# Optimization experiments

Measured on AMD Instinct MI355X. Metric: run time of the kernel, lower is better.

## Reference

```python
import jax, jax.numpy as jnp
import numpy as np
from jax import lax

N = 1_000_000   # nodes
E = 16_000_000  # edges
K1, K2, K3 = 100_000, 10_000, 2_500  # ceil(ratio*n) per pooling stage
EPS = 1e-5


def cgconv(x, src, dst, edge_attr, edge_valid, Wf, bf, Ws, bs, gamma, beta, num_nodes):
    # z_ij = [x_i, x_j, e_ij]  (PyG: i = target = dst, j = source = src)
    z = jnp.concatenate([x[dst], x[src], edge_attr], axis=-1)          # [E,3]
    m = jax.nn.sigmoid(z @ Wf + bf) * jax.nn.softplus(z @ Ws + bs)     # [E,1]
    m = m * edge_valid[:, None].astype(m.dtype)
    aggr = jax.ops.segment_sum(m, dst, num_segments=num_nodes)         # [n,1]
    # BatchNorm1d (training-mode batch stats, biased var), then residual
    mean = aggr.mean(axis=0)
    var = aggr.var(axis=0)
    bn = gamma * (aggr - mean) / jnp.sqrt(var + EPS) + beta
    return bn + x


def topk_pool(x, src, dst, edge_attr, edge_valid, w, k, num_nodes):
    # Original torch code broadcasts x[N,1]*w[C] -> sum(-1) == x*sum(w); tanh nonlinearity.
    score = jnp.tanh(x[:, 0] * jnp.sum(w) / jnp.linalg.norm(w))        # [n]
    top_scores, perm = lax.top_k(score, k)
    x_new = x[perm] * top_scores[:, None]
    mask = jnp.zeros((num_nodes,), bool).at[perm].set(True)
    new_idx = jnp.zeros((num_nodes,), jnp.int32).at[perm].set(jnp.arange(k, dtype=jnp.int32))
    ev = edge_valid & mask[src] & mask[dst]
    return x_new, new_idx[src], new_idx[dst], edge_attr, ev


def setup_inputs() -> dict:
    key = jax.random.key(0)
    ks = jax.random.split(key, 24)
    d = {}
    d["x"] = jax.random.normal(ks[0], (N, 1), jnp.float32)
    d["edge_attr"] = jax.random.uniform(ks[1], (E, 1), jnp.float32)
    d["src"] = jax.random.randint(ks[2], (E,), 0, N, jnp.int32)
    d["dst"] = jax.random.randint(ks[3], (E,), 0, N, jnp.int32)
    d["batch"] = jnp.zeros((N,), jnp.int32)
    p = lambda k, shp: jax.random.normal(k, shp, jnp.float32) * 0.1
    d["Wf1"], d["bf1"] = p(ks[4], (3, 1)), p(ks[5], (1,))
    d["Ws1"], d["bs1"] = p(ks[6], (3, 1)), p(ks[7], (1,))
    d["g1"], d["be1"] = jnp.ones((1,), jnp.float32), jnp.zeros((1,), jnp.float32)
    d["Wf2"], d["bf2"] = p(ks[8], (3, 1)), p(ks[9], (1,))
    d["Ws2"], d["bs2"] = p(ks[10], (3, 1)), p(ks[11], (1,))
    d["g2"], d["be2"] = jnp.ones((1,), jnp.float32), jnp.zeros((1,), jnp.float32)
    d["pw1"] = p(ks[12], (800,))
    d["pw2"] = p(ks[13], (80,))
    d["pw3"] = p(ks[14], (8,))
    d["Wl1"], d["bl1"] = p(ks[15], (1, 8)), p(ks[16], (8,))
    d["Wl2"], d["bl2"] = p(ks[17], (8, 2)), p(ks[18], (2,))
    return d


def reference(x, edge_attr, Wf1, bf1, Ws1, bs1, g1, be1, Wf2, bf2, Ws2, bs2, g2, be2,
              pw1, pw2, pw3, Wl1, bl1, Wl2, bl2, src, dst, batch):
    ev = jnp.ones((E,), bool)
    x = cgconv(x, src, dst, edge_attr, ev, Wf1, bf1, Ws1, bs1, g1, be1, N)
    x, s, dd, ea, ev = topk_pool(x, src, dst, edge_attr, ev, pw1, K1, N)
    x = cgconv(x, s, dd, ea, ev, Wf2, bf2, Ws2, bs2, g2, be2, K1)
    x, s, dd, ea, ev = topk_pool(x, s, dd, ea, ev, pw2, K2, K1)
    x, s, dd, ea, ev = topk_pool(x, s, dd, ea, ev, pw3, K3, K2)
    h = jax.nn.relu(x @ Wl1 + bl1)
    # dropout is identity in eval/reference mode
    return jax.nn.log_softmax(h @ Wl2 + bl2, axis=1)
```

## Files before the change

kernel.cpp:

```cpp
#include <hip/hip_runtime.h>
#include <math.h>

#define CHUNK 4096
#define NB2   256
#define BSH   12
#define CAP   24
#define CAPW  49
#define FG    16
#define RND   1024
#define EPB   32768

__device__ __forceinline__ float sigmoidf_(float x) {
    if (x >= 0.0f) { float e = expf(-x); return 1.0f / (1.0f + e); }
    float e = expf(x); return e / (1.0f + e);
}
__device__ __forceinline__ float softplusf_(float x) {
    return fmaxf(x, 0.0f) + log1pf(expf(-fabsf(x)));
}
__device__ __forceinline__ unsigned key_desc(float f) {
    unsigned u = __float_as_uint(f);
    unsigned ka = (u & 0x80000000u) ? ~u : (u | 0x80000000u);
    return ~ka;
}
__device__ __forceinline__ float edge_m(float xd, float xs, float a,
                                        float wf0, float wf1, float wf2, float b0,
                                        float ws0, float ws1, float ws2, float b1) {
    float f = xd * wf0 + xs * wf1 + a * wf2 + b0;
    float g = xd * ws0 + xs * ws1 + a * ws2 + b1;
    return sigmoidf_(f) * softplusf_(g);
}

__global__ void k_consts(const float* __restrict__ pw1, const float* __restrict__ pw2,
                         const float* __restrict__ pw3, float* __restrict__ consts,
                         int n1, int n2, int n3) {
    const float* w; int n;
    if (blockIdx.x == 0)      { w = pw1; n = n1; }
    else if (blockIdx.x == 1) { w = pw2; n = n2; }
    else                      { w = pw3; n = n3; }
    __shared__ float s1[256], s2[256];
    float a = 0.f, b = 0.f;
    for (int i = threadIdx.x; i < n; i += 256) { float v = w[i]; a += v; b += v * v; }
    s1[threadIdx.x] = a; s2[threadIdx.x] = b; __syncthreads();
    for (int o = 128; o > 0; o >>= 1) {
        if (threadIdx.x < o) { s1[threadIdx.x] += s1[threadIdx.x + o]; s2[threadIdx.x] += s2[threadIdx.x + o]; }
        __syncthreads();
    }
    if (threadIdx.x == 0) consts[blockIdx.x] = s1[0] / sqrtf(s2[0]);
}

__global__ void __launch_bounds__(256) k_ehist2(const int* __restrict__ dst,
                                                unsigned* __restrict__ hist,
                                                int e0, int e1) {
    __shared__ unsigned h[NB2];
    int t = threadIdx.x;
    h[t] = 0;
    __syncthreads();
    int cs = e0 + blockIdx.x * EPB;
    int ce = cs + EPB; if (ce > e1) ce = e1;
    for (int eb = cs; eb < ce; eb += RND) {
        int i = eb + t * 4;
        if (eb + RND <= ce) {
            int4 d4 = *(const int4*)(dst + i);
            atomicAdd(&h[((unsigned)d4.x) >> BSH], 1u);
            atomicAdd(&h[((unsigned)d4.y) >> BSH], 1u);
            atomicAdd(&h[((unsigned)d4.z) >> BSH], 1u);
            atomicAdd(&h[((unsigned)d4.w) >> BSH], 1u);
        } else {
            #pragma unroll
            for (int j = 0; j < 4; ++j)
                if (i + j < ce) atomicAdd(&h[((unsigned)dst[i + j]) >> BSH], 1u);
        }
    }
    __syncthreads();
    hist[(size_t)blockIdx.x * NB2 + t] = h[t];
}

__global__ void k_scanA(const unsigned* __restrict__ hist, unsigned* __restrict__ offs,
                        unsigned* __restrict__ tot, int G) {
    int d = blockIdx.x, ND = gridDim.x, t = threadIdx.x;
    __shared__ unsigned s[256];
    unsigned carry = 0;
    for (int tile = 0; tile * 256 < G; ++tile) {
        int g = tile * 256 + t;
        unsigned v = (g < G) ? hist[(size_t)g * ND + d] : 0u;
        s[t] = v; __syncthreads();
        for (int o = 1; o < 256; o <<= 1) {
            unsigned u = (t >= o) ? s[t - o] : 0u;
            __syncthreads();
            s[t] += u; __syncthreads();
        }
        if (g < G) offs[(size_t)g * ND + d] = s[t] - v + carry;
        unsigned tl = s[255]; __syncthreads();
        carry += tl;
    }
    if (t == 0) tot[d] = carry;
}

__global__ void k_scanB(const unsigned* __restrict__ tot, unsigned* __restrict__ base,
                        int ND, unsigned rmask) {
    __shared__ unsigned s[256];
    int t = threadIdx.x;
    unsigned carry = 0;
    for (int tile = 0; tile * 256 < ND; ++tile) {
        int d = tile * 256 + t;
        unsigned v = (d < ND) ? ((tot[d] + rmask) & ~rmask) : 0u;
        s[t] = v; __syncthreads();
        for (int o = 1; o < 256; o <<= 1) {
            unsigned u = (t >= o) ? s[t - o] : 0u;
            __syncthreads();
            s[t] += u; __syncthreads();
        }
        if (d < ND) base[d] = s[t] - v + carry;
        unsigned tl = s[255]; __syncthreads();
        carry += tl;
    }
    if (t == 0) base[ND] = carry;
}

__global__ void __launch_bounds__(256) k_part(
        const float* __restrict__ x, const float* __restrict__ ea,
        const int* __restrict__ src, const int* __restrict__ dst,
        const float* __restrict__ Wf, const float* __restrict__ bf,
        const float* __restrict__ Ws, const float* __restrict__ bs,
        const unsigned* __restrict__ offs, const unsigned* __restrict__ binBase,
        uint2* __restrict__ rec, int e0, int e1) {
    __shared__ unsigned stage[NB2 * CAPW];
    __shared__ unsigned gcur[NB2], fil[NB2];
    int t = threadIdx.x;
    gcur[t] = binBase[t] + offs[(size_t)blockIdx.x * NB2 + t];
    fil[t] = 0;
    __syncthreads();
    int cs = e0 + blockIdx.x * EPB;
    int ce = cs + EPB; if (ce > e1) ce = e1;
    float wf0 = Wf[0], wf1 = Wf[1], wf2 = Wf[2], b0 = bf[0];
    float ws0 = Ws[0], ws1 = Ws[1], ws2 = Ws[2], b1 = bs[0];
    for (int rb = cs; rb < ce; rb += RND) {
        int s4[4], d4[4]; float a4[4]; bool vl[4];
        int eb = rb + t * 4;
        if (rb + RND <= ce) {
            int4 sv = *(const int4*)(src + eb);
            int4 dv = *(const int4*)(dst + eb);
            float4 av = *(const float4*)(ea + eb);
            s4[0]=sv.x; s4[1]=sv.y; s4[2]=sv.z; s4[3]=sv.w;
            d4[0]=dv.x; d4[1]=dv.y; d4[2]=dv.z; d4[3]=dv.w;
            a4[0]=av.x; a4[1]=av.y; a4[2]=av.z; a4[3]=av.w;
            vl[0]=vl[1]=vl[2]=vl[3]=true;
        } else {
            #pragma unroll
            for (int j = 0; j < 4; ++j) {
                int e = eb + j;
                vl[j] = e < ce;
                s4[j] = vl[j] ? src[e] : 0;
                d4[j] = vl[j] ? dst[e] : 0;
                a4[j] = vl[j] ? ea[e]  : 0.f;
            }
        }
        #pragma unroll
        for (int j = 0; j < 4; ++j) {
            if (!vl[j]) continue;
            int d = d4[j];
            float m = edge_m(x[d], x[s4[j]], a4[j], wf0, wf1, wf2, b0, ws0, ws1, ws2, b1);
            unsigned bin = ((unsigned)d) >> BSH;
            unsigned dl  = (unsigned)(d & ((1 << BSH) - 1));
            unsigned slot = atomicAdd(&fil[bin], 1u);
            if (slot < CAP) {
                stage[bin * CAPW + 2 * slot]     = __float_as_uint(m);
                stage[bin * CAPW + 2 * slot + 1] = dl;
            } else {
                rec[gcur[bin] + slot] = make_uint2(__float_as_uint(m), dl);
            }
        }
        __syncthreads();
        {
            unsigned c = fil[t], g = gcur[t];
            unsigned* st = &stage[t * CAPW];
            if (c > CAP) {
                for (unsigned k = 0; k < CAP; ++k)
                    rec[g + k] = make_uint2(st[2 * k], st[2 * k + 1]);
                gcur[t] = g + c; fil[t] = 0;
            } else {
                unsigned ngrp = c >> 4;
                if (ngrp) {
                    unsigned nfl = ngrp << 4;
                    for (unsigned k = 0; k < nfl; ++k)
                        rec[g + k] = make_uint2(st[2 * k], st[2 * k + 1]);
                    unsigned rem = c - nfl;
                    for (unsigned k = 0; k < rem; ++k) {
                        st[2 * k]     = st[2 * (nfl + k)];
                        st[2 * k + 1] = st[2 * (nfl + k) + 1];
                    }
                    gcur[t] = g + nfl; fil[t] = rem;
                }
            }
        }
        __syncthreads();
    }
    {
        unsigned c = fil[t], g = gcur[t];
        unsigned* st = &stage[t * CAPW];
        unsigned cc = c < CAP ? c : CAP;
        for (unsigned k = 0; k < cc; ++k)
            rec[g + k] = make_uint2(st[2 * k], st[2 * k + 1]);
    }
}

__global__ void __launch_bounds__(256) k_aggr2(
        const uint2* __restrict__ rec, const unsigned* __restrict__ base,
        const unsigned* __restrict__ tot, float* __restrict__ aggr,
        float* __restrict__ stats, int N, int accumulate, int doStats) {
    __shared__ float acc[1 << BSH];
    int t = threadIdx.x, b = blockIdx.x;
    for (int i = t; i < (1 << BSH); i += 256) acc[i] = 0.f;
    __syncthreads();
    unsigned lo = base[b], hi = lo + tot[b];
    for (unsigned i = lo + t; i < hi; i += 256) {
        uint2 r = rec[i];
        atomicAdd(&acc[r.y], __uint_as_float(r.x));
    }
    __syncthreads();
    int nb = b << BSH;
    float s = 0.f, q = 0.f;
    for (int i = t; i < (1 << BSH); i += 256) {
        int node = nb + i;
        if (node < N) {
            float v = acc[i];
            if (accumulate) v += aggr[node];
            aggr[node] = v;
            if (doStats) { s += v; q += v * v; }
        }
    }
    if (doStats) {
        __shared__ float s1[256], s2[256];
        s1[t] = s; s2[t] = q; __syncthreads();
        for (int o = 128; o > 0; o >>= 1) {
            if (t < o) { s1[t] += s1[t + o]; s2[t] += s2[t + o]; }
            __syncthreads();
        }
        if (t == 0) { atomicAdd(&stats[0], s1[0]); atomicAdd(&stats[1], s2[0]); }
    }
}

__global__ void k_conv1(const float* __restrict__ x, const float* __restrict__ ea,
                        const int* __restrict__ src, const int* __restrict__ dst,
                        const float* __restrict__ Wf, const float* __restrict__ bf,
                        const float* __restrict__ Ws, const float* __restrict__ bs,
                        float* __restrict__ aggr, int E) {
    int e = blockIdx.x * blockDim.x + threadIdx.x;
    if (e >= E) return;
    int s = src[e], d = dst[e];
    atomicAdd(&aggr[d], edge_m(x[d], x[s], ea[e], Wf[0], Wf[1], Wf[2], bf[0],
                               Ws[0], Ws[1], Ws[2], bs[0]));
}

__global__ void k_conv2(const float* __restrict__ x2, const float* __restrict__ ea,
                        const int* __restrict__ src, const int* __restrict__ dst,
                        const int* __restrict__ nidx,
                        const float* __restrict__ Wf, const float* __restrict__ bf,
                        const float* __restrict__ Ws, const float* __restrict__ bs,
                        float* __restrict__ aggr, int E) {
    int e = blockIdx.x * blockDim.x + threadIdx.x;
    if (e >= E) return;
    int nd = nidx[dst[e]];
    if (nd < 0) return;
    int ns = nidx[src[e]];
    if (ns < 0) return;
    atomicAdd(&aggr[nd], edge_m(x2[nd], x2[ns], ea[e], Wf[0], Wf[1], Wf[2], bf[0],
                                Ws[0], Ws[1], Ws[2], bs[0]));
}

__global__ void k_stats(const float* __restrict__ a, int n, float* __restrict__ stats) {
    float s = 0.f, q = 0.f;
    int stride = gridDim.x * blockDim.x;
    for (int i = blockIdx.x * blockDim.x + threadIdx.x; i < n; i += stride) {
        float v = a[i]; s += v; q += v * v;
    }
    __shared__ float s1[256], s2[256];
    s1[threadIdx.x] = s; s2[threadIdx.x] = q; __syncthreads();
    for (int o = 128; o > 0; o >>= 1) {
        if (threadIdx.x < o) { s1[threadIdx.x] += s1[threadIdx.x + o]; s2[threadIdx.x] += s2[threadIdx.x + o]; }
        __syncthreads();
    }
    if (threadIdx.x == 0) { atomicAdd(&stats[0], s1[0]); atomicAdd(&stats[1], s2[0]); }
}

__global__ void k_bn(const float* __restrict__ aggr, const float* __restrict__ xin,
                     const float* __restrict__ stats, const float* __restrict__ g,
                     const float* __restrict__ be, float* __restrict__ xout,
                     int n, float invn, const float* __restrict__ consts, int ci,
                     unsigned* __restrict__ keys, unsigned* __restrict__ vals) {
    int i = blockIdx.x * blockDim.x + threadIdx.x;
    if (i >= n) return;
    float mean = stats[0] * invn;
    float var  = stats[1] * invn - mean * mean;
    float inv  = 1.0f / sqrtf(var + 1e-5f);
    float v = g[0] * (aggr[i] - mean) * inv + be[0] + xin[i];
    xout[i] = v;
    if (keys) {
        float s = tanhf(v * consts[ci]);
        keys[i] = key_desc(s);
        vals[i] = (unsigned)i;
    }
}

__global__ void k_hist(const unsigned* __restrict__ keys, unsigned* __restrict__ hist,
                       int n, int shift) {
    __shared__ unsigned h[256];
    h[threadIdx.x] = 0;
    __syncthreads();
    int base = blockIdx.x * CHUNK;
    int end = base + CHUNK; if (end > n) end = n;
    for (int i = base + threadIdx.x; i < end; i += 256)
        atomicAdd(&h[(keys[i] >> shift) & 255u], 1u);
    __syncthreads();
    hist[blockIdx.x * 256 + threadIdx.x] = h[threadIdx.x];
}

__global__ void __launch_bounds__(256) k_scatter(const unsigned* __restrict__ keys,
                                                 const unsigned* __restrict__ vals,
                                                 unsigned* __restrict__ okeys,
                                                 unsigned* __restrict__ ovals,
                                                 const unsigned* __restrict__ offs,
                                                 const unsigned* __restrict__ base_,
                                                 int n, int shift) {
    __shared__ unsigned run[256];
    __shared__ unsigned offl[256];
    __shared__ unsigned wcnt[4][256];
    __shared__ unsigned wpre[4][256];
    int t = threadIdx.x;
    int wave = t >> 6, lane = t & 63;
    run[t] = 0;
    offl[t] = offs[(size_t)blockIdx.x * 256 + t] + base_[t];
    __syncthreads();
    int cbase = blockIdx.x * CHUNK;
    const int GROUPS = CHUNK / 256;
    for (int gix = 0; gix < GROUPS; ++gix) {
        int i = cbase + gix * 256 + t;
        bool active = i < n;
        unsigned k = active ? keys[i] : 0u;
        unsigned v = active ? vals[i] : 0u;
        unsigned d = (k >> shift) & 255u;
        unsigned long long amask = __ballot(active);
        unsigned long long bb[8];
        #pragma unroll
        for (int bit = 0; bit < 8; ++bit) bb[bit] = __ballot(active && ((d >> bit) & 1u));
        unsigned long long m = amask;
        #pragma unroll
        for (int bit = 0; bit < 8; ++bit) m &= ((d >> bit) & 1u) ? bb[bit] : ~bb[bit];
        unsigned rk = (unsigned)__popcll(m & ((1ull << lane) - 1ull));
        #pragma unroll
        for (int j = 0; j < 4; ++j) {
            unsigned dd = (unsigned)lane + j * 64u;
            unsigned long long mm = amask;
            #pragma unroll
            for (int bit = 0; bit < 8; ++bit) mm &= ((dd >> bit) & 1u) ? bb[bit] : ~bb[bit];
            wcnt[wave][dd] = (unsigned)__popcll(mm);
        }
        __syncthreads();
        {
            unsigned r = run[t];
            unsigned c0 = wcnt[0][t], c1 = wcnt[1][t], c2 = wcnt[2][t], c3 = wcnt[3][t];
            wpre[0][t] = r;
            wpre[1][t] = r + c0;
            wpre[2][t] = r + c0 + c1;
            wpre[3][t] = r + c0 + c1 + c2;
            run[t] = r + c0 + c1 + c2 + c3;
        }
        __syncthreads();
        if (active) {
            unsigned pos = offl[d] + wpre[wave][d] + rk;
            okeys[pos] = k;
            ovals[pos] = v;
        }
    }
}

__global__ void k_pool(const unsigned* __restrict__ perm, const float* __restrict__ xin,
                       const float* __restrict__ consts, int ci,
                       float* __restrict__ xout, int* __restrict__ newidx, int k,
                       unsigned* __restrict__ okeys, unsigned* __restrict__ ovals, int nci) {
    int r = blockIdx.x * blockDim.x + threadIdx.x;
    if (r >= k) return;
    unsigned p = perm[r];
    float xv = xin[p];
    float s = tanhf(xv * consts[ci]);
    float o = xv * s;
    xout[r] = o;
    if (newidx) newidx[p] = r;
    if (okeys) {
        float s2 = tanhf(o * consts[nci]);
        okeys[r] = key_desc(s2);
        ovals[r] = (unsigned)r;
    }
}

__global__ void k_mlp(const float* __restrict__ x5, const float* __restrict__ Wl1,
                      const float* __restrict__ bl1, const float* __restrict__ Wl2,
                      const float* __restrict__ bl2, float* __restrict__ out, int n) {
    int i = blockIdx.x * blockDim.x + threadIdx.x;
    if (i >= n) return;
    float xv = x5[i];
    float l0 = bl2[0], l1 = bl2[1];
    #pragma unroll
    for (int j = 0; j < 8; ++j) {
        float h = fmaxf(xv * Wl1[j] + bl1[j], 0.0f);
        l0 += h * Wl2[2 * j];
        l1 += h * Wl2[2 * j + 1];
    }
    float mx = fmaxf(l0, l1);
    float lse = mx + logf(expf(l0 - mx) + expf(l1 - mx));
    out[2 * i]     = l0 - lse;
    out[2 * i + 1] = l1 - lse;
}

static void sort_pairs(hipStream_t stream, unsigned* kA, unsigned* vA,
                       unsigned* kB, unsigned* vB, unsigned* hist, unsigned* offs,
                       unsigned* tot, unsigned* base, int n) {
    int G = (n + CHUNK - 1) / CHUNK;
    unsigned *ki = kA, *vi = vA, *ko = kB, *vo = vB;
    for (int p = 0; p < 4; ++p) {
        int shift = p * 8;
        k_hist<<<G, 256, 0, stream>>>(ki, hist, n, shift);
        k_scanA<<<256, 256, 0, stream>>>(hist, offs, tot, G);
        k_scanB<<<1, 256, 0, stream>>>(tot, base, 256, 0u);
        k_scatter<<<G, 256, 0, stream>>>(ki, vi, ko, vo, offs, base, n, shift);
        unsigned* t;
        t = ki; ki = ko; ko = t;
        t = vi; vi = vo; vo = t;
    }
}

extern "C" void kernel_launch(void* const* d_in, const int* in_sizes, int n_in,
                              void* d_out, int out_size, void* d_ws, size_t ws_size,
                              hipStream_t stream) {
    const float* x   = (const float*)d_in[0];
    const float* ea  = (const float*)d_in[1];
    const int*   src = (const int*)d_in[2];
    const int*   dst = (const int*)d_in[3];
    const float *Wf1 = (const float*)d_in[5],  *bf1 = (const float*)d_in[6];
    const float *Ws1 = (const float*)d_in[7],  *bs1 = (const float*)d_in[8];
    const float *g1  = (const float*)d_in[9],  *be1 = (const float*)d_in[10];
    const float *Wf2 = (const float*)d_in[11], *bf2 = (const float*)d_in[12];
    const float *Ws2 = (const float*)d_in[13], *bs2 = (const float*)d_in[14];
    const float *g2  = (const float*)d_in[15], *be2 = (const float*)d_in[16];
    const float *pw1 = (const float*)d_in[17], *pw2 = (const float*)d_in[18], *pw3 = (const float*)d_in[19];
    const float *Wl1 = (const float*)d_in[20], *bl1 = (const float*)d_in[21];
    const float *Wl2 = (const float*)d_in[22], *bl2 = (const float*)d_in[23];

    const int N  = in_sizes[0];
    const int E  = in_sizes[1];
    const int K1 = 100000, K2 = 10000, K3 = 2500;

    size_t off = 0;
    auto alloc = [&](size_t bytes) { size_t o = off; off = (off + bytes + 255) & ~(size_t)255; return o; };
    char* ws = (char*)d_ws;
    size_t o_x1    = alloc((size_t)N * 4);
    size_t o_nidx  = alloc((size_t)N * 4);
    size_t o_stats = alloc(256);
    size_t o_const = alloc(256);
    size_t o_tot   = alloc(4096);
    size_t o_base  = alloc(8192);
    size_t o_x2    = alloc((size_t)K1 * 4);
    size_t o_x3    = alloc((size_t)K1 * 4);
    size_t o_ag2   = alloc((size_t)K1 * 4);
    size_t o_x4    = alloc((size_t)K2 * 4);
    size_t o_x5    = alloc((size_t)K3 * 4);
    size_t o_ag1   = alloc((size_t)N * 4);
    size_t o_arena = off;

    int G1 = (N + CHUNK - 1) / CHUNK;
    size_t s_kA = 0;
    size_t s_vA = s_kA + (((size_t)N * 4 + 255) & ~(size_t)255);
    size_t s_kB = s_vA + (((size_t)N * 4 + 255) & ~(size_t)255);
    size_t s_vB = s_kB + (((size_t)N * 4 + 255) & ~(size_t)255);
    size_t s_h  = s_vB + (((size_t)N * 4 + 255) & ~(size_t)255);
    size_t s_o  = s_h  + (((size_t)G1 * 256 * 4 + 255) & ~(size_t)255);
    size_t sortSz = s_o + (size_t)G1 * 256 * 4;

    int H = 0, Eh = 0;
    size_t p_rec = 0, p_eh = 0, p_eo = 0;
    for (int h = 1; h <= 8; h <<= 1) {
        int eh_ = (E + h - 1) / h;
        eh_ = (eh_ + RND - 1) & ~(RND - 1);
        int gc_ = (eh_ + EPB - 1) / EPB;
        size_t recB = (((size_t)(eh_ + NB2 * FG) * 8) + 255) & ~(size_t)255;
        size_t ehB  = (((size_t)gc_ * NB2 * 4) + 255) & ~(size_t)255;
        size_t eoB  = (((size_t)gc_ * NB2 * 4) + 255) & ~(size_t)255;
        size_t partSz = recB + ehB + eoB;
        size_t arenaSz = partSz > sortSz ? partSz : sortSz;
        if (o_arena + arenaSz <= ws_size && N <= (NB2 << BSH)) {
            H = h; Eh = eh_;
            p_rec = 0; p_eh = p_rec + recB; p_eo = p_eh + ehB;
            break;
        }
    }

    float*    x1     = (float*)(ws + o_x1);
    int*      nidx   = (int*)(ws + o_nidx);
    float*    stats  = (float*)(ws + o_stats);
    float*    consts = (float*)(ws + o_const);
    unsigned* tot    = (unsigned*)(ws + o_tot);
    unsigned* base   = (unsigned*)(ws + o_base);
    float*    x2     = (float*)(ws + o_x2);
    float*    x3     = (float*)(ws + o_x3);
    float*    aggr2  = (float*)(ws + o_ag2);
    float*    x4     = (float*)(ws + o_x4);
    float*    x5     = (float*)(ws + o_x5);
    float*    aggr1  = (float*)(ws + o_ag1);
    unsigned* kA     = (unsigned*)(ws + o_arena + s_kA);
    unsigned* vA     = (unsigned*)(ws + o_arena + s_vA);
    unsigned* kB     = (unsigned*)(ws + o_arena + s_kB);
    unsigned* vB     = (unsigned*)(ws + o_arena + s_vB);
    unsigned* hist   = (unsigned*)(ws + o_arena + s_h);
    unsigned* offs   = (unsigned*)(ws + o_arena + s_o);

    hipMemsetAsync(nidx, 0xFF, (size_t)N * 4, stream);
    hipMemsetAsync(stats, 0, 64, stream);
    hipMemsetAsync(aggr2, 0, (size_t)K1 * 4, stream);

    k_consts<<<3, 256, 0, stream>>>(pw1, pw2, pw3, consts,
                                    in_sizes[17], in_sizes[18], in_sizes[19]);

    if (H > 0) {
        uint2*    rec = (uint2*)(ws + o_arena + p_rec);
        unsigned* eh  = (unsigned*)(ws + o_arena + p_eh);
        unsigned* eo  = (unsigned*)(ws + o_arena + p_eo);
        int NBN = (N + (1 << BSH) - 1) >> BSH;
        for (int h = 0; h < H; ++h) {
            int e0 = h * Eh;
            int e1 = e0 + Eh; if (e1 > E) e1 = E;
            if (e0 >= e1) break;
            int GCh = (e1 - e0 + EPB - 1) / EPB;
            k_ehist2<<<GCh, 256, 0, stream>>>(dst, eh, e0, e1);
            k_scanA<<<NB2, 256, 0, stream>>>(eh, eo, tot, GCh);
            k_scanB<<<1, 256, 0, stream>>>(tot, base, NB2, (unsigned)(FG - 1));
            k_part<<<GCh, 256, 0, stream>>>(x, ea, src, dst, Wf1, bf1, Ws1, bs1,
                                            eo, base, rec, e0, e1);
            k_aggr2<<<NBN, 256, 0, stream>>>(rec, base, tot, aggr1, stats, N,
                                             h > 0, h == H - 1 ? 1 : 0);
        }
    } else {
        hipMemsetAsync(aggr1, 0, (size_t)N * 4, stream);
        k_conv1<<<(E + 255) / 256, 256, 0, stream>>>(x, ea, src, dst, Wf1, bf1, Ws1, bs1, aggr1, E);
        k_stats<<<1024, 256, 0, stream>>>(aggr1, N, stats);
    }
    k_bn<<<(N + 255) / 256, 256, 0, stream>>>(aggr1, x, stats, g1, be1, x1, N, 1.0f / (float)N,
                                              consts, 0, kA, vA);

    sort_pairs(stream, kA, vA, kB, vB, hist, offs, tot, base, N);
    k_pool<<<(K1 + 255) / 256, 256, 0, stream>>>(vA, x1, consts, 0, x2, nidx, K1,
                                                 (unsigned*)nullptr, (unsigned*)nullptr, 0);

    k_conv2<<<(E + 255) / 256, 256, 0, stream>>>(x2, ea, src, dst, nidx, Wf2, bf2, Ws2, bs2, aggr2, E);
    k_stats<<<256, 256, 0, stream>>>(aggr2, K1, stats + 2);
    k_bn<<<(K1 + 255) / 256, 256, 0, stream>>>(aggr2, x2, stats + 2, g2, be2, x3, K1, 1.0f / (float)K1,
                                               consts, 1, kA, vA);

    sort_pairs(stream, kA, vA, kB, vB, hist, offs, tot, base, K1);
    k_pool<<<(K2 + 255) / 256, 256, 0, stream>>>(vA, x3, consts, 1, x4, (int*)nullptr, K2,
                                                 kB, vB, 2);

    sort_pairs(stream, kB, vB, kA, vA, hist, offs, tot, base, K2);
    k_pool<<<(K3 + 255) / 256, 256, 0, stream>>>(vB, x4, consts, 2, x5, (int*)nullptr, K3,
                                                 (unsigned*)nullptr, (unsigned*)nullptr, 0);

    k_mlp<<<(K3 + 255) / 256, 256, 0, stream>>>(x5, Wl1, bl1, Wl2, bl2, (float*)d_out, K3);
}
```

Measured before the change: 931.9 us.

## Use nontemporal loads, vectorize conv2/hist, fuse final sort with pool and MLP

Streaming edge loads in the histogram, partition, aggregation and conv2 kernels now use nontemporal loads so they pollute the cache less. conv2 handles four edges per thread with a vectorized dst load, k_hist unrolls its loads four per thread, and EPB is halved to give more blocks. The last 10k-element radix sort, the top-k pool and the MLP are merged into one single-block 1024-thread kernel to cut launch overhead. The single-block sort runs serially on one CU, and the smaller EPB adds more histogram and partition blocks.

Result: faster. 902.3 us (-3.2%).

```diff
diff --git a/kernel.cpp b/kernel.cpp
--- a/kernel.cpp
+++ b/kernel.cpp
@@ -8,7 +8,14 @@
 #define CAPW  49
 #define FG    16
 #define RND   1024
-#define EPB   32768
+#define EPB   16384
+
+typedef int      i32x4 __attribute__((ext_vector_type(4)));
+typedef float    f32x4 __attribute__((ext_vector_type(4)));
+typedef unsigned u32x2 __attribute__((ext_vector_type(2)));
+
+__device__ __forceinline__ i32x4 ntld4i(const int* p)   { return __builtin_nontemporal_load((const i32x4*)p); }
+__device__ __forceinline__ f32x4 ntld4f(const float* p) { return __builtin_nontemporal_load((const f32x4*)p); }
 
 __device__ __forceinline__ float sigmoidf_(float x) {
     if (x >= 0.0f) { float e = expf(-x); return 1.0f / (1.0f + e); }
@@ -60,7 +67,7 @@
     for (int eb = cs; eb < ce; eb += RND) {
         int i = eb + t * 4;
         if (eb + RND <= ce) {
-            int4 d4 = *(const int4*)(dst + i);
+            i32x4 d4 = ntld4i(dst + i);
             atomicAdd(&h[((unsigned)d4.x) >> BSH], 1u);
             atomicAdd(&h[((unsigned)d4.y) >> BSH], 1u);
             atomicAdd(&h[((unsigned)d4.z) >> BSH], 1u);
@@ -138,9 +145,9 @@
         int s4[4], d4[4]; float a4[4]; bool vl[4];
         int eb = rb + t * 4;
         if (rb + RND <= ce) {
-            int4 sv = *(const int4*)(src + eb);
-            int4 dv = *(const int4*)(dst + eb);
-            float4 av = *(const float4*)(ea + eb);
+            i32x4 sv = ntld4i(src + eb);
+            i32x4 dv = ntld4i(dst + eb);
+            f32x4 av = ntld4f(ea + eb);
             s4[0]=sv.x; s4[1]=sv.y; s4[2]=sv.z; s4[3]=sv.w;
             d4[0]=dv.x; d4[1]=dv.y; d4[2]=dv.z; d4[3]=dv.w;
             a4[0]=av.x; a4[1]=av.y; a4[2]=av.z; a4[3]=av.w;
@@ -214,7 +221,7 @@
     __syncthreads();
     unsigned lo = base[b], hi = lo + tot[b];
     for (unsigned i = lo + t; i < hi; i += 256) {
-        uint2 r = rec[i];
+        u32x2 r = __builtin_nontemporal_load((const u32x2*)&rec[i]);
         atomicAdd(&acc[r.y], __uint_as_float(r.x));
     }
     __syncthreads();
@@ -252,20 +259,37 @@
                                Ws[0], Ws[1], Ws[2], bs[0]));
 }
 
-__global__ void k_conv2(const float* __restrict__ x2, const float* __restrict__ ea,
-                        const int* __restrict__ src, const int* __restrict__ dst,
-                        const int* __restrict__ nidx,
-                        const float* __restrict__ Wf, const float* __restrict__ bf,
-                        const float* __restrict__ Ws, const float* __restrict__ bs,
-                        float* __restrict__ aggr, int E) {
-    int e = blockIdx.x * blockDim.x + threadIdx.x;
-    if (e >= E) return;
-    int nd = nidx[dst[e]];
-    if (nd < 0) return;
-    int ns = nidx[src[e]];
-    if (ns < 0) return;
-    atomicAdd(&aggr[nd], edge_m(x2[nd], x2[ns], ea[e], Wf[0], Wf[1], Wf[2], bf[0],
-                                Ws[0], Ws[1], Ws[2], bs[0]));
+__global__ void __launch_bounds__(256) k_conv2(
+        const float* __restrict__ x2, const float* __restrict__ ea,
+        const int* __restrict__ src, const int* __restrict__ dst,
+        const int* __restrict__ nidx,
+        const float* __restrict__ Wf, const float* __restrict__ bf,
+        const float* __restrict__ Ws, const float* __restrict__ bs,
+        float* __restrict__ aggr, int E) {
+    int base = (blockIdx.x * 256 + threadIdx.x) * 4;
+    if (base >= E) return;
+    float wf0 = Wf[0], wf1 = Wf[1], wf2 = Wf[2], b0 = bf[0];
+    float ws0 = Ws[0], ws1 = Ws[1], ws2 = Ws[2], b1 = bs[0];
+    int d4[4]; int cnt;
+    if (base + 4 <= E) {
+        i32x4 dv = ntld4i(dst + base);
+        d4[0]=dv.x; d4[1]=dv.y; d4[2]=dv.z; d4[3]=dv.w;
+        cnt = 4;
+    } else {
+        cnt = E - base;
+        for (int j = 0; j < cnt; ++j) d4[j] = dst[base + j];
+    }
+    #pragma unroll
+    for (int j = 0; j < 4; ++j) {
+        if (j >= cnt) break;
+        int nd = nidx[d4[j]];
+        if (nd < 0) continue;
+        int sv = __builtin_nontemporal_load(src + base + j);
+        int ns = nidx[sv];
+        if (ns < 0) continue;
+        float a = __builtin_nontemporal_load(ea + base + j);
+        atomicAdd(&aggr[nd], edge_m(x2[nd], x2[ns], a, wf0, wf1, wf2, b0, ws0, ws1, ws2, b1));
+    }
 }
 
 __global__ void k_stats(const float* __restrict__ a, int n, float* __restrict__ stats) {
@@ -305,14 +329,28 @@
 __global__ void k_hist(const unsigned* __restrict__ keys, unsigned* __restrict__ hist,
                        int n, int shift) {
     __shared__ unsigned h[256];
-    h[threadIdx.x] = 0;
+    int t = threadIdx.x;
+    h[t] = 0;
     __syncthreads();
     int base = blockIdx.x * CHUNK;
-    int end = base + CHUNK; if (end > n) end = n;
-    for (int i = base + threadIdx.x; i < end; i += 256)
-        atomicAdd(&h[(keys[i] >> shift) & 255u], 1u);
-    __syncthreads();
-    hist[blockIdx.x * 256 + threadIdx.x] = h[threadIdx.x];
+    if (base + CHUNK <= n) {
+        #pragma unroll
+        for (int it = 0; it < CHUNK / 1024; ++it) {
+            int i = base + it * 1024 + t * 4;
+            const unsigned* p = keys + i;
+            unsigned k0 = p[0], k1 = p[1], k2 = p[2], k3 = p[3];
+            atomicAdd(&h[(k0 >> shift) & 255u], 1u);
+            atomicAdd(&h[(k1 >> shift) & 255u], 1u);
+            atomicAdd(&h[(k2 >> shift) & 255u], 1u);
+            atomicAdd(&h[(k3 >> shift) & 255u], 1u);
+        }
+    } else {
+        int end = n;
+        for (int i = base + t; i < end; i += 256)
+            atomicAdd(&h[(keys[i] >> shift) & 255u], 1u);
+    }
+    __syncthreads();
+    hist[blockIdx.x * 256 + t] = h[t];
 }
 
 __global__ void __launch_bounds__(256) k_scatter(const unsigned* __restrict__ keys,
@@ -393,23 +431,100 @@
     }
 }
 
-__global__ void k_mlp(const float* __restrict__ x5, const float* __restrict__ Wl1,
-                      const float* __restrict__ bl1, const float* __restrict__ Wl2,
-                      const float* __restrict__ bl2, float* __restrict__ out, int n) {
-    int i = blockIdx.x * blockDim.x + threadIdx.x;
-    if (i >= n) return;
-    float xv = x5[i];
-    float l0 = bl2[0], l1 = bl2[1];
-    #pragma unroll
-    for (int j = 0; j < 8; ++j) {
-        float h = fmaxf(xv * Wl1[j] + bl1[j], 0.0f);
-        l0 += h * Wl2[2 * j];
-        l1 += h * Wl2[2 * j + 1];
-    }
-    float mx = fmaxf(l0, l1);
-    float lse = mx + logf(expf(l0 - mx) + expf(l1 - mx));
-    out[2 * i]     = l0 - lse;
-    out[2 * i + 1] = l1 - lse;
+__global__ void __launch_bounds__(1024) k_smallsort(
+        unsigned* __restrict__ kIn, unsigned* __restrict__ vIn,
+        unsigned* __restrict__ kTmp, unsigned* __restrict__ vTmp,
+        int n, int k3, const float* __restrict__ xin,
+        const float* __restrict__ consts, int ci,
+        const float* __restrict__ Wl1, const float* __restrict__ bl1,
+        const float* __restrict__ Wl2, const float* __restrict__ bl2,
+        float* __restrict__ out) {
+    __shared__ unsigned hist[256], sc[256], run[256], offl[256];
+    __shared__ unsigned wcnt[16][256];
+    __shared__ unsigned wpre[16][256];
+    int t = threadIdx.x;
+    int wave = t >> 6, lane = t & 63;
+    unsigned *ki = kIn, *vi = vIn, *ko = kTmp, *vo = vTmp;
+    for (int p = 0; p < 4; ++p) {
+        int shift = p * 8;
+        if (t < 256) hist[t] = 0;
+        __syncthreads();
+        for (int i = t; i < n; i += 1024)
+            atomicAdd(&hist[(ki[i] >> shift) & 255u], 1u);
+        __syncthreads();
+        if (t < 256) sc[t] = hist[t];
+        __syncthreads();
+        for (int o = 1; o < 256; o <<= 1) {
+            unsigned u = 0;
+            if (t < 256 && t >= o) u = sc[t - o];
+            __syncthreads();
+            if (t < 256) sc[t] += u;
+            __syncthreads();
+        }
+        if (t < 256) { offl[t] = sc[t] - hist[t]; run[t] = 0; }
+        __syncthreads();
+        int G = (n + 1023) / 1024;
+        for (int gix = 0; gix < G; ++gix) {
+            int i = gix * 1024 + t;
+            bool active = i < n;
+            unsigned k = active ? ki[i] : 0u;
+            unsigned v = active ? vi[i] : 0u;
+            unsigned d = (k >> shift) & 255u;
+            unsigned long long amask = __ballot(active);
+            unsigned long long bb[8];
+            #pragma unroll
+            for (int bit = 0; bit < 8; ++bit) bb[bit] = __ballot(active && ((d >> bit) & 1u));
+            unsigned long long m = amask;
+            #pragma unroll
+            for (int bit = 0; bit < 8; ++bit) m &= ((d >> bit) & 1u) ? bb[bit] : ~bb[bit];
+            unsigned rk = (unsigned)__popcll(m & ((1ull << lane) - 1ull));
+            #pragma unroll
+            for (int j = 0; j < 4; ++j) {
+                unsigned dd = (unsigned)lane + j * 64u;
+                unsigned long long mm = amask;
+                #pragma unroll
+                for (int bit = 0; bit < 8; ++bit) mm &= ((dd >> bit) & 1u) ? bb[bit] : ~bb[bit];
+                wcnt[wave][dd] = (unsigned)__popcll(mm);
+            }
+            __syncthreads();
+            if (t < 256) {
+                unsigned acc = run[t];
+                #pragma unroll
+                for (int w2 = 0; w2 < 16; ++w2) { wpre[w2][t] = acc; acc += wcnt[w2][t]; }
+                run[t] = acc;
+            }
+            __syncthreads();
+            if (active) {
+                unsigned pos = offl[d] + wpre[wave][d] + rk;
+                ko[pos] = k;
+                vo[pos] = v;
+            }
+            __syncthreads();
+        }
+        unsigned* tp;
+        tp = ki; ki = ko; ko = tp;
+        tp = vi; vi = vo; vo = tp;
+        __syncthreads();
+    }
+    float c = consts[ci];
+    float b20 = bl2[0], b21 = bl2[1];
+    for (int r = t; r < k3; r += 1024) {
+        unsigned pidx = vIn[r];
+        float xv = xin[pidx];
+        float s = tanhf(xv * c);
+        float o = xv * s;
+        float l0 = b20, l1 = b21;
+        #pragma unroll
+        for (int j = 0; j < 8; ++j) {
+            float h = fmaxf(o * Wl1[j] + bl1[j], 0.0f);
+            l0 += h * Wl2[2 * j];
+            l1 += h * Wl2[2 * j + 1];
+        }
+        float mx = fmaxf(l0, l1);
+        float lse = mx + logf(expf(l0 - mx) + expf(l1 - mx));
+        out[2 * r]     = l0 - lse;
+        out[2 * r + 1] = l1 - lse;
+    }
 }
 
 static void sort_pairs(hipStream_t stream, unsigned* kA, unsigned* vA,
@@ -504,7 +619,6 @@
     float*    x3     = (float*)(ws + o_x3);
     float*    aggr2  = (float*)(ws + o_ag2);
     float*    x4     = (float*)(ws + o_x4);
-    float*    x5     = (float*)(ws + o_x5);
     float*    aggr1  = (float*)(ws + o_ag1);
     unsigned* kA     = (unsigned*)(ws + o_arena + s_kA);
     unsigned* vA     = (unsigned*)(ws + o_arena + s_vA);
@@ -550,7 +664,8 @@
     k_pool<<<(K1 + 255) / 256, 256, 0, stream>>>(vA, x1, consts, 0, x2, nidx, K1,
                                                  (unsigned*)nullptr, (unsigned*)nullptr, 0);
 
-    k_conv2<<<(E + 255) / 256, 256, 0, stream>>>(x2, ea, src, dst, nidx, Wf2, bf2, Ws2, bs2, aggr2, E);
+    k_conv2<<<(E / 4 + 255) / 256, 256, 0, stream>>>(x2, ea, src, dst, nidx,
+                                                     Wf2, bf2, Ws2, bs2, aggr2, E);
     k_stats<<<256, 256, 0, stream>>>(aggr2, K1, stats + 2);
     k_bn<<<(K1 + 255) / 256, 256, 0, stream>>>(aggr2, x2, stats + 2, g2, be2, x3, K1, 1.0f / (float)K1,
                                                consts, 1, kA, vA);
@@ -559,9 +674,6 @@
     k_pool<<<(K2 + 255) / 256, 256, 0, stream>>>(vA, x3, consts, 1, x4, (int*)nullptr, K2,
                                                  kB, vB, 2);
 
-    sort_pairs(stream, kB, vB, kA, vA, hist, offs, tot, base, K2);
-    k_pool<<<(K3 + 255) / 256, 256, 0, stream>>>(vB, x4, consts, 2, x5, (int*)nullptr, K3,
-                                                 (unsigned*)nullptr, (unsigned*)nullptr, 0);
-
-    k_mlp<<<(K3 + 255) / 256, 256, 0, stream>>>(x5, Wl1, bl1, Wl2, bl2, (float*)d_out, K3);
-}
+    k_smallsort<<<1, 1024, 0, stream>>>(kB, vB, kA, vA, K2, K3, x4, consts, 2,
+                                        Wl1, bl1, Wl2, bl2, (float*)d_out);
+}
```
